# Performance work log

Hardware: AMD Instinct MI355X
Metric: run time of the kernel (lower is better)

Reference implementation:

```python
import jax, jax.numpy as jnp
import numpy as np

N_NODES = 100000
N_EDGES = 1600000
NUM_FEATURES = 32
EDGE_DIM = 8
GAT_DIM = 16
HEADS = 4
HID = GAT_DIM * HEADS  # 64
OUT_DIM = 2
NUM_GRAPHS = 64
NEG_SLOPE = 0.2


def setup_inputs() -> dict:
    key = jax.random.key(0)
    ks = jax.random.split(key, 24)
    g = lambda k, shp, fan: jax.random.normal(k, shp, jnp.float32) * (1.0 / np.sqrt(fan))
    inp = {
        'x': jax.random.normal(ks[0], (N_NODES, NUM_FEATURES), jnp.float32),
        'edge_index': jax.random.randint(ks[1], (2, N_EDGES), 0, N_NODES, jnp.int64),
        'edge_attr': jax.random.normal(ks[2], (N_EDGES, EDGE_DIM), jnp.float32),
        'batch': jnp.sort(jax.random.randint(ks[3], (N_NODES,), 0, NUM_GRAPHS, jnp.int64)),
        # input GATConv params (PyG: lin bias-free, att_* of shape [H,C], bias [H*C])
        'W0': g(ks[4], (NUM_FEATURES, HID), NUM_FEATURES),
        'att_src0': g(ks[5], (HEADS, GAT_DIM), GAT_DIM),
        'att_dst0': g(ks[6], (HEADS, GAT_DIM), GAT_DIM),
        'We0': g(ks[7], (EDGE_DIM, HID), EDGE_DIM),
        'att_e0': g(ks[8], (HEADS, GAT_DIM), GAT_DIM),
        'b0': jnp.zeros((HID,), jnp.float32),
        # 2 hidden GATConv layers, stacked on a leading layer axis
        'Wh': g(ks[9], (2, HID, HID), HID),
        'att_src_h': g(ks[10], (2, HEADS, GAT_DIM), GAT_DIM),
        'att_dst_h': g(ks[11], (2, HEADS, GAT_DIM), GAT_DIM),
        'We_h': g(ks[12], (2, EDGE_DIM, HID), EDGE_DIM),
        'att_e_h': g(ks[13], (2, HEADS, GAT_DIM), GAT_DIM),
        'bh': jnp.zeros((2, HID), jnp.float32),
        # MLP head
        'fc1_w': g(ks[14], (HID, 2 * GAT_DIM), HID),
        'fc1_b': jnp.zeros((2 * GAT_DIM,), jnp.float32),
        'fc2_w': g(ks[15], (2 * GAT_DIM, OUT_DIM), 2 * GAT_DIM),
        'fc2_b': jnp.zeros((OUT_DIM,), jnp.float32),
    }
    return inp


def _gat_conv(x, src, dst, ea, W, a_s, a_d, We, a_e, b, n_nodes):
    # x: [N, Fin] -> out: [N, H*C]
    xp = (x @ W).reshape(n_nodes, HEADS, GAT_DIM)
    al_s = jnp.einsum('nhc,hc->nh', xp, a_s)            # per-node src logits
    al_d = jnp.einsum('nhc,hc->nh', xp, a_d)
    ep = (ea @ We).reshape(-1, HEADS, GAT_DIM)
    al_e = jnp.einsum('ehc,hc->eh', ep, a_e)
    alpha = jax.nn.leaky_relu(al_s[src] + al_d[dst] + al_e, NEG_SLOPE)  # [E,H]
    m = jax.ops.segment_max(alpha, dst, num_segments=n_nodes)
    m = jnp.where(jnp.isfinite(m), m, 0.0)              # nodes with no in-edges
    ex = jnp.exp(alpha - m[dst])
    den = jax.ops.segment_sum(ex, dst, num_segments=n_nodes)
    coef = ex / (den[dst] + 1e-16)                      # segment softmax over dst
    out = jax.ops.segment_sum(xp[src] * coef[..., None], dst, num_segments=n_nodes)
    return out.reshape(n_nodes, HID) + b


def _forward(x, edge_index, edge_attr, batch, W0, att_src0, att_dst0, We0, att_e0,
             b0, Wh, att_src_h, att_dst_h, We_h, att_e_h, bh, fc1_w, fc1_b, fc2_w, fc2_b):
    n = x.shape[0]
    src, dst = edge_index[0], edge_index[1]
    # PyG add_self_loops(fill_value='mean'): self-loop attr = mean of incoming edge attrs
    cnt = jax.ops.segment_sum(jnp.ones((src.shape[0],), x.dtype), dst, num_segments=n)
    mean_attr = jax.ops.segment_sum(edge_attr, dst, num_segments=n) / jnp.clip(cnt, 1.0)[:, None]
    loop = jnp.arange(n, dtype=src.dtype)
    src_sl = jnp.concatenate([src, loop])
    dst_sl = jnp.concatenate([dst, loop])
    ea_sl = jnp.concatenate([edge_attr, mean_attr], axis=0)

    h = _gat_conv(x, src_sl, dst_sl, ea_sl, W0, att_src0, att_dst0, We0, att_e0, b0, n)
    h = jax.nn.relu(h)
    for i in range(2):  # source has `x - F.relu(x)` (no-op): no ReLU between hidden layers
        h = _gat_conv(h, src_sl, dst_sl, ea_sl, Wh[i], att_src_h[i], att_dst_h[i],
                      We_h[i], att_e_h[i], bh[i], n)
    # global_mean_pool over graphs
    ones = jnp.ones((n,), h.dtype)
    gcnt = jax.ops.segment_sum(ones, batch, num_segments=NUM_GRAPHS)
    pooled = jax.ops.segment_sum(h, batch, num_segments=NUM_GRAPHS) / jnp.clip(gcnt, 1.0)[:, None]
    y = jax.nn.relu(pooled @ fc1_w + fc1_b)
    return y @ fc2_w + fc2_b


def reference(x, edge_index, edge_attr, batch, W0, att_src0, att_dst0, We0, att_e0,
              b0, Wh, att_src_h, att_dst_h, We_h, att_e_h, bh, fc1_w, fc1_b, fc2_w, fc2_b):
    return _forward(x, edge_index, edge_attr, batch, W0, att_src0, att_dst0, We0, att_e0,
                    b0, Wh, att_src_h, att_dst_h, We_h, att_e_h, bh, fc1_w, fc1_b, fc2_w, fc2_b)
```

## Files before the change

kernel.cpp:

```cpp
#include <hip/hip_runtime.h>
#include <hip/hip_bf16.h>
#include <hip/hip_fp16.h>

#define N_NODES 100000
#define N_EDGES 1600000
#define E_SL (N_EDGES + N_NODES)
#define HID 64
#define NUM_GRAPHS 64
#define NEG_SLOPE 0.2f
#define SCAN_CHUNK 1024
#define SCAN_NB ((N_NODES + SCAN_CHUNK - 1) / SCAN_CHUNK)
#define ROW_W 8
#define XP_NODES_PER_BLK 16
#define POOL_NODES_PER_BLK 256
#define BUILD_NB (N_EDGES / 128)
#define XP0_NB ((N_NODES + 15) / 16)


__global__ void hist_kernel(const int* __restrict__ ei, int* __restrict__ cnt,
                            int* __restrict__ rank) {
    int e = blockIdx.x * blockDim.x + threadIdx.x;
    if (e >= N_EDGES) return;
    rank[e] = atomicAdd(&cnt[ei[N_EDGES + e]], 1);
}

__global__ void scan_local_kernel(const int* __restrict__ cnt, int* __restrict__ row_ptr,
                                  int* __restrict__ bsum) {
    __shared__ int s[256];
    int t = threadIdx.x;
    int base = blockIdx.x * SCAN_CHUNK + t * 4;
    int v[4]; int sum = 0;
    #pragma unroll
    for (int i = 0; i < 4; ++i) {
        int idx = base + i;
        v[i] = (idx < N_NODES) ? cnt[idx] + 1 : 0;
        sum += v[i];
    }
    s[t] = sum;
    __syncthreads();
    for (int off = 1; off < 256; off <<= 1) {
        int x = (t >= off) ? s[t - off] : 0;
        __syncthreads();
        s[t] += x;
        __syncthreads();
    }
    int run = s[t] - sum;
    #pragma unroll
    for (int i = 0; i < 4; ++i) {
        int idx = base + i;
        if (idx < N_NODES) row_ptr[idx] = run;
        run += v[i];
    }
    if (t == 255) bsum[blockIdx.x] = s[255];
}

__global__ void scan_bsum_kernel(int* __restrict__ bsum) {
    if (threadIdx.x != 0) return;
    int acc = 0;
    for (int i = 0; i < SCAN_NB; ++i) { int v = bsum[i]; bsum[i] = acc; acc += v; }
}

__global__ void scan_add_kernel(int* __restrict__ row_ptr, const int* __restrict__ bsum) {
    int i = blockIdx.x * blockDim.x + threadIdx.x;
    if (i > N_NODES) return;
    if (i == N_NODES) row_ptr[i] = E_SL;
    else row_ptr[i] += bsum[i >> 10];
}

__global__ void weff_all_kernel(const float* __restrict__ We0, const float* __restrict__ ae0,
                                const float* __restrict__ Weh, const float* __restrict__ aeh,
                                float* __restrict__ weff) {
    int t = threadIdx.x;
    if (t >= 96) return;
    int layer = t >> 5, r = t & 31;
    int dd = r >> 2, h = r & 3;
    const float* We = (layer == 0) ? We0 : Weh + (size_t)(layer - 1) * 8 * 64;
    const float* ae = (layer == 0) ? ae0 : aeh + (size_t)(layer - 1) * 64;
    float s = 0.f;
    #pragma unroll
    for (int c = 0; c < 16; ++c) s += We[dd * 64 + h * 16 + c] * ae[h * 16 + c];
    weff[layer * 32 + dd * 4 + h] = s;
}

__global__ __launch_bounds__(256) void build_xp0_kernel(
    const int* __restrict__ ei, const float* __restrict__ ea,
    const int* __restrict__ row_ptr, const int* __restrict__ rank,
    const float* __restrict__ weff, unsigned int* __restrict__ ale_csr,
    const float* __restrict__ x, const float* __restrict__ W0,
    const float* __restrict__ a_s, const float* __restrict__ a_d,
    __half* __restrict__ xp, float* __restrict__ als, float* __restrict__ ald) {
    int b = blockIdx.x;
    int g = b / 3, r3 = b - g * 3;
    if (r3 == 2) {
        int wave = threadIdx.x >> 6, lane = threadIdx.x & 63;
        float wcol[32];
        #pragma unroll
        for (int k = 0; k < 32; ++k) wcol[k] = W0[k * 64 + lane];
        float asl = a_s[lane], adl = a_d[lane];
        int n0 = g * XP_NODES_PER_BLK + wave * 4;
        #pragma unroll 1
        for (int ni = 0; ni < 4; ++ni) {
            int n = n0 + ni;
            if (n >= N_NODES) return;
            const float* xr = x + (size_t)n * 32;
            float a0 = 0.f, a1 = 0.f, a2 = 0.f, a3 = 0.f;
            #pragma unroll
            for (int k = 0; k < 32; k += 4) {
                float4 xv = *(const float4*)(xr + k);
                a0 += xv.x * wcol[k];     a1 += xv.y * wcol[k + 1];
                a2 += xv.z * wcol[k + 2]; a3 += xv.w * wcol[k + 3];
            }
            float acc = (a0 + a1) + (a2 + a3);
            xp[(size_t)n * 64 + lane] = __float2half(acc);
            float ps = acc * asl, pd = acc * adl;
            #pragma unroll
            for (int mk = 8; mk >= 1; mk >>= 1) {
                ps += __shfl_xor(ps, mk, 16);
                pd += __shfl_xor(pd, mk, 16);
            }
            if ((lane & 15) == 0) {
                als[(size_t)n * 4 + (lane >> 4)] = ps;
                ald[(size_t)n * 4 + (lane >> 4)] = pd;
            }
        }
        return;
    }
    int build_b = g * 2 + r3;
    int e = build_b * 128 + (threadIdx.x >> 1);
    int q = threadIdx.x & 1;
    int d = ei[N_EDGES + e];
    float4 a = *((const float4*)(ea + (size_t)e * 8) + q);
    float o0 = __shfl_xor(a.x, 1), o1 = __shfl_xor(a.y, 1);
    float o2 = __shfl_xor(a.z, 1), o3 = __shfl_xor(a.w, 1);
    float av[8];
    av[0] = q ? o0 : a.x;  av[1] = q ? o1 : a.y;
    av[2] = q ? o2 : a.z;  av[3] = q ? o3 : a.w;
    av[4] = q ? a.x : o0;  av[5] = q ? a.y : o1;
    av[6] = q ? a.z : o2;  av[7] = q ? a.w : o3;
    unsigned int w[4];
    if (q == 0) {
        float al[8];
        #pragma unroll
        for (int l = 0; l < 2; ++l) {
            #pragma unroll
            for (int h = 0; h < 4; ++h) {
                float s = 0.f;
                #pragma unroll
                for (int j = 0; j < 8; ++j) s += av[j] * weff[l * 32 + j * 4 + h];
                al[l * 4 + h] = s;
            }
        }
        __half2 p0 = __floats2half2_rn(al[0], al[1]);
        __half2 p1 = __floats2half2_rn(al[2], al[3]);
        __half2 p2 = __floats2half2_rn(al[4], al[5]);
        __half2 p3 = __floats2half2_rn(al[6], al[7]);
        w[0] = *(unsigned int*)&p0; w[1] = *(unsigned int*)&p1;
        w[2] = *(unsigned int*)&p2; w[3] = *(unsigned int*)&p3;
    } else {
        float al[4];
        #pragma unroll
        for (int h = 0; h < 4; ++h) {
            float s = 0.f;
            #pragma unroll
            for (int j = 0; j < 8; ++j) s += av[j] * weff[64 + j * 4 + h];
            al[h] = s;
        }
        __half2 p0 = __floats2half2_rn(al[0], al[1]);
        __half2 p1 = __floats2half2_rn(al[2], al[3]);
        w[0] = *(unsigned int*)&p0; w[1] = *(unsigned int*)&p1;
        w[2] = (unsigned int)ei[e];
        w[3] = 0u;
    }
    int pos = row_ptr[d] + rank[e];
    *(uint4*)(ale_csr + (size_t)pos * ROW_W + q * 4) =
        make_uint4(w[0], w[1], w[2], w[3]);
}

__global__ void mean_ea_kernel(const int* __restrict__ row_ptr,
                               unsigned int* __restrict__ ale_csr) {
    int idx = blockIdx.x * blockDim.x + threadIdx.x;
    if (idx >= N_NODES * 2) return;
    int n = idx >> 1, part = idx & 1;
    int start = row_ptr[n], last = row_ptr[n + 1] - 1;
    float inv = 1.f / fmaxf((float)(last - start), 1.f);
    if (part == 0) {
        float s[8] = {0.f, 0.f, 0.f, 0.f, 0.f, 0.f, 0.f, 0.f};
        for (int pos = start; pos < last; ++pos) {
            uint4 v = *(const uint4*)(ale_csr + (size_t)pos * ROW_W);
            float2 f0 = __half22float2(*(const __half2*)&v.x);
            float2 f1 = __half22float2(*(const __half2*)&v.y);
            float2 f2 = __half22float2(*(const __half2*)&v.z);
            float2 f3 = __half22float2(*(const __half2*)&v.w);
            s[0] += f0.x; s[1] += f0.y; s[2] += f1.x; s[3] += f1.y;
            s[4] += f2.x; s[5] += f2.y; s[6] += f3.x; s[7] += f3.y;
        }
        __half2 p0 = __floats2half2_rn(s[0] * inv, s[1] * inv);
        __half2 p1 = __floats2half2_rn(s[2] * inv, s[3] * inv);
        __half2 p2 = __floats2half2_rn(s[4] * inv, s[5] * inv);
        __half2 p3 = __floats2half2_rn(s[6] * inv, s[7] * inv);
        *(uint4*)(ale_csr + (size_t)last * ROW_W) =
            make_uint4(*(unsigned int*)&p0, *(unsigned int*)&p1,
                       *(unsigned int*)&p2, *(unsigned int*)&p3);
    } else {
        float s[4] = {0.f, 0.f, 0.f, 0.f};
        for (int pos = start; pos < last; ++pos) {
            uint2 v = *(const uint2*)(ale_csr + (size_t)pos * ROW_W + 4);
            float2 f0 = __half22float2(*(const __half2*)&v.x);
            float2 f1 = __half22float2(*(const __half2*)&v.y);
            s[0] += f0.x; s[1] += f0.y; s[2] += f1.x; s[3] += f1.y;
        }
        __half2 p0 = __floats2half2_rn(s[0] * inv, s[1] * inv);
        __half2 p1 = __floats2half2_rn(s[2] * inv, s[3] * inv);
        uint4 w = make_uint4(*(unsigned int*)&p0, *(unsigned int*)&p1,
                             (unsigned int)n, 0u);
        *(uint4*)(ale_csr + (size_t)last * ROW_W + 4) = w;
    }
}


template <int FIN>
__global__ __launch_bounds__(64) void xp_kernel(
    const float* __restrict__ xin, const float* __restrict__ W,
    const float* __restrict__ a_s, const float* __restrict__ a_d,
    __half* __restrict__ xp, float* __restrict__ als, float* __restrict__ ald) {
    int lane = threadIdx.x;
    float wcol[FIN];
    #pragma unroll
    for (int k = 0; k < FIN; ++k) wcol[k] = W[k * 64 + lane];
    float asl = a_s[lane], adl = a_d[lane];
    int n0 = blockIdx.x * XP_NODES_PER_BLK;
    #pragma unroll 1
    for (int ni = 0; ni < XP_NODES_PER_BLK; ++ni) {
        int n = n0 + ni;
        if (n >= N_NODES) return;
        const float* xr = xin + (size_t)n * FIN;
        float a0 = 0.f, a1 = 0.f, a2 = 0.f, a3 = 0.f;
        #pragma unroll
        for (int k = 0; k < FIN; k += 4) {
            float4 xv = *(const float4*)(xr + k);
            a0 += xv.x * wcol[k];     a1 += xv.y * wcol[k + 1];
            a2 += xv.z * wcol[k + 2]; a3 += xv.w * wcol[k + 3];
        }
        float acc = (a0 + a1) + (a2 + a3);
        xp[(size_t)n * 64 + lane] = __float2half(acc);
        float ps = acc * asl, pd = acc * adl;
        #pragma unroll
        for (int mk = 8; mk >= 1; mk >>= 1) {
            ps += __shfl_xor(ps, mk, 16);
            pd += __shfl_xor(pd, mk, 16);
        }
        if ((lane & 15) == 0) {
            als[(size_t)n * 4 + (lane >> 4)] = ps;
            ald[(size_t)n * 4 + (lane >> 4)] = pd;
        }
    }
}

__global__ __launch_bounds__(256) void gat_node_kernel(
    const int* __restrict__ row_ptr, const unsigned int* __restrict__ ale_csr,
    const float* __restrict__ als, const float* __restrict__ ald,
    const __half* __restrict__ xp, int layer,
    float* __restrict__ out, const float* __restrict__ bias, int relu_flag) {
    __shared__ float exl[4 * 256];
    __shared__ int   coll[4 * 64];
    int wave = threadIdx.x >> 6, lane = threadIdx.x & 63;
    int node = blockIdx.x * 4 + wave;
    if (node >= N_NODES) return;
    int start = row_ptr[node], end = row_ptr[node + 1];
    int deg = end - start;
    int wb = wave * 64, wb4 = wave * 256;
    int cq = lane & 15;
    int eg = lane >> 4;
    int hv = cq >> 2;

    float4 ad4 = *(const float4*)(ald + (size_t)node * 4);

    float4 acc4 = make_float4(0.f, 0.f, 0.f, 0.f);
    float csum = 0.f;

    for (int base = 0; base < deg; base += 64) {
        int cnt = min(64, deg - base);
        float ex0 = 0.f, ex1 = 0.f, ex2 = 0.f, ex3 = 0.f;
        int s = 0;
        if (lane < cnt) {
            const unsigned int* row = ale_csr + (size_t)(start + base + lane) * ROW_W;
            uint2 alew = *(const uint2*)(row + 2 * layer);
            s = (int)row[6];
            float2 e01 = __half22float2(*(const __half2*)&alew.x);
            float2 e23 = __half22float2(*(const __half2*)&alew.y);
            float4 as4 = *(const float4*)(als + (size_t)s * 4);
            float v0 = as4.x + ad4.x + e01.x;
            float v1 = as4.y + ad4.y + e01.y;
            float v2 = as4.z + ad4.z + e23.x;
            float v3 = as4.w + ad4.w + e23.y;
            ex0 = expf((v0 >= 0.f) ? v0 : NEG_SLOPE * v0);
            ex1 = expf((v1 >= 0.f) ? v1 : NEG_SLOPE * v1);
            ex2 = expf((v2 >= 0.f) ? v2 : NEG_SLOPE * v2);
            ex3 = expf((v3 >= 0.f) ? v3 : NEG_SLOPE * v3);
        }
        *(float4*)(exl + wb4 + lane * 4) = make_float4(ex0, ex1, ex2, ex3);
        coll[wb + lane] = s;
        const float* exw = exl + wb4 + hv;
        int cntUp = (cnt + 15) & ~15;
        for (int j = eg; j < cntUp; j += 16) {
            int s0 = coll[wb + j],     s1 = coll[wb + j + 4];
            int s2 = coll[wb + j + 8], s3 = coll[wb + j + 12];
            float c0 = exw[(j) * 4],      c1 = exw[(j + 4) * 4];
            float c2 = exw[(j + 8) * 4],  c3 = exw[(j + 12) * 4];
            uint2 x0 = *(const uint2*)(xp + (size_t)s0 * 64 + cq * 4);
            uint2 x1 = *(const uint2*)(xp + (size_t)s1 * 64 + cq * 4);
            uint2 x2 = *(const uint2*)(xp + (size_t)s2 * 64 + cq * 4);
            uint2 x3 = *(const uint2*)(xp + (size_t)s3 * 64 + cq * 4);
            float2 f00 = __half22float2(*(const __half2*)&x0.x);
            float2 f01 = __half22float2(*(const __half2*)&x0.y);
            float2 f10 = __half22float2(*(const __half2*)&x1.x);
            float2 f11 = __half22float2(*(const __half2*)&x1.y);
            float2 f20 = __half22float2(*(const __half2*)&x2.x);
            float2 f21 = __half22float2(*(const __half2*)&x2.y);
            float2 f30 = __half22float2(*(const __half2*)&x3.x);
            float2 f31 = __half22float2(*(const __half2*)&x3.y);
            acc4.x += c0 * f00.x + c1 * f10.x + c2 * f20.x + c3 * f30.x;
            acc4.y += c0 * f00.y + c1 * f10.y + c2 * f20.y + c3 * f30.y;
            acc4.z += c0 * f01.x + c1 * f11.x + c2 * f21.x + c3 * f31.x;
            acc4.w += c0 * f01.y + c1 * f11.y + c2 * f21.y + c3 * f31.y;
            csum   += c0 + c1 + c2 + c3;
        }
    }
    #pragma unroll
    for (int mk = 16; mk < 64; mk <<= 1) {
        acc4.x += __shfl_xor(acc4.x, mk);
        acc4.y += __shfl_xor(acc4.y, mk);
        acc4.z += __shfl_xor(acc4.z, mk);
        acc4.w += __shfl_xor(acc4.w, mk);
        csum   += __shfl_xor(csum, mk);
    }
    if (eg == 0) {
        float inv = 1.f / (csum + 1e-16f);
        float4 b4 = *(const float4*)(bias + cq * 4);
        float4 v;
        v.x = acc4.x * inv + b4.x;
        v.y = acc4.y * inv + b4.y;
        v.z = acc4.z * inv + b4.z;
        v.w = acc4.w * inv + b4.w;
        if (relu_flag) {
            v.x = fmaxf(v.x, 0.f); v.y = fmaxf(v.y, 0.f);
            v.z = fmaxf(v.z, 0.f); v.w = fmaxf(v.w, 0.f);
        }
        *(float4*)(out + (size_t)node * 64 + cq * 4) = v;
    }
}

__global__ void pool_kernel(const float* __restrict__ h, const int* __restrict__ batch,
                            float* __restrict__ pooled) {
    int base = blockIdx.x * POOL_NODES_PER_BLK;
    int tid = threadIdx.x;
    int c = tid & 63, r = tid >> 6;
    float acc = 0.f;
    int curg = -1;
    for (int i = r; i < POOL_NODES_PER_BLK; i += 4) {
        int n = base + i;
        if (n >= N_NODES) break;
        int g = batch[n];
        if (g != curg) {
            if (curg >= 0) atomicAdd(&pooled[curg * 64 + c], acc);
            curg = g; acc = 0.f;
        }
        acc += h[(size_t)n * 64 + c];
    }
    if (curg >= 0) atomicAdd(&pooled[curg * 64 + c], acc);
}

__global__ void mlp_kernel(const float* __restrict__ pooled, const int* __restrict__ batch,
                           const float* __restrict__ w1, const float* __restrict__ b1,
                           const float* __restrict__ w2, const float* __restrict__ b2,
                           float* __restrict__ y) {
    int g = blockIdx.x, t = threadIdx.x;
    __shared__ float p[64], f1[32];
    __shared__ float invc_s;
    if (t == 0) {
        int lo = 0, hi = N_NODES;
        while (lo < hi) { int mid = (lo + hi) >> 1; if (batch[mid] < g) lo = mid + 1; else hi = mid; }
        int start = lo;
        hi = N_NODES;
        while (lo < hi) { int mid = (lo + hi) >> 1; if (batch[mid] < g + 1) lo = mid + 1; else hi = mid; }
        invc_s = 1.f / fmaxf((float)(lo - start), 1.f);
    }
    __syncthreads();
    p[t] = pooled[g * 64 + t] * invc_s;
    __syncthreads();
    if (t < 32) {
        float a = b1[t];
        #pragma unroll
        for (int k = 0; k < 64; ++k) a += p[k] * w1[k * 32 + t];
        f1[t] = fmaxf(a, 0.f);
    }
    __syncthreads();
    if (t < 2) {
        float a = b2[t];
        #pragma unroll
        for (int k = 0; k < 32; ++k) a += f1[k] * w2[k * 2 + t];
        y[g * 2 + t] = a;
    }
}

extern "C" void kernel_launch(void* const* d_in, const int* in_sizes, int n_in,
                              void* d_out, int out_size, void* d_ws, size_t ws_size,
                              hipStream_t stream) {
    const float* x    = (const float*)d_in[0];
    const int*   ei   = (const int*)d_in[1];
    const float* ea   = (const float*)d_in[2];
    const int*   batch= (const int*)d_in[3];
    const float* W0   = (const float*)d_in[4];
    const float* as0  = (const float*)d_in[5];
    const float* ad0  = (const float*)d_in[6];
    const float* We0  = (const float*)d_in[7];
    const float* ae0  = (const float*)d_in[8];
    const float* b0   = (const float*)d_in[9];
    const float* Wh   = (const float*)d_in[10];
    const float* ash  = (const float*)d_in[11];
    const float* adh  = (const float*)d_in[12];
    const float* Weh  = (const float*)d_in[13];
    const float* aeh  = (const float*)d_in[14];
    const float* bh   = (const float*)d_in[15];
    const float* w1   = (const float*)d_in[16];
    const float* b1   = (const float*)d_in[17];
    const float* w2   = (const float*)d_in[18];
    const float* b2   = (const float*)d_in[19];
    float* out = (float*)d_out;

    char* wsb = (char*)d_ws;
    size_t off = 0;
    auto alloc = [&](size_t bytes) { char* p = wsb + off; off += (bytes + 255) & ~(size_t)255; return p; };
    int*          row_ptr = (int*)alloc((size_t)(N_NODES + 1) * 4);
    unsigned int* ale_csr = (unsigned int*)alloc((size_t)E_SL * ROW_W * 4);
    float*        als     = (float*)alloc((size_t)N_NODES * 4 * 4);
    float*        ald     = (float*)alloc((size_t)N_NODES * 4 * 4);
    float*        weff    = (float*)alloc(3 * 32 * 4);
    float*        pooled  = (float*)alloc((size_t)NUM_GRAPHS * 64 * 4);
    __half*       bufA    = (__half*)alloc((size_t)N_NODES * 64 * 2);
    float*        bufB    = (float*)alloc((size_t)N_NODES * 64 * 4);
    int* cnt  = (int*)bufB;
    int* bsum = cnt + N_NODES;
    int* rank = bsum + ((SCAN_NB + 63) & ~63);

    weff_all_kernel<<<1, 128, 0, stream>>>(We0, ae0, Weh, aeh, weff);
    hipMemsetAsync(cnt, 0, (size_t)N_NODES * 4, stream);
    hist_kernel<<<(N_EDGES + 255) / 256, 256, 0, stream>>>(ei, cnt, rank);
    scan_local_kernel<<<SCAN_NB, 256, 0, stream>>>(cnt, row_ptr, bsum);
    scan_bsum_kernel<<<1, 64, 0, stream>>>(bsum);
    scan_add_kernel<<<(N_NODES + 256) / 256, 256, 0, stream>>>(row_ptr, bsum);
    build_xp0_kernel<<<BUILD_NB + XP0_NB, 256, 0, stream>>>(
        ei, ea, row_ptr, rank, weff, ale_csr,
        x, W0, as0, ad0, bufA, als, ald);
    mean_ea_kernel<<<(N_NODES * 2 + 255) / 256, 256, 0, stream>>>(row_ptr, ale_csr);

    for (int layer = 0; layer < 3; ++layer) {
        const float *bb;
        int relu_flag = (layer == 0);
        if (layer == 0) {
            bb = b0;
        } else {
            int i = layer - 1;
            const float* W   = Wh  + (size_t)i * 64 * 64;
            const float* as_ = ash + (size_t)i * 64;
            const float* ad_ = adh + (size_t)i * 64;
            bb  = bh  + (size_t)i * 64;
            int xpgrid = (N_NODES + XP_NODES_PER_BLK - 1) / XP_NODES_PER_BLK;
            xp_kernel<64><<<xpgrid, 64, 0, stream>>>(bufB, W, as_, ad_, bufA, als, ald);
        }
        gat_node_kernel<<<(N_NODES + 3) / 4, 256, 0, stream>>>(
            row_ptr, ale_csr, als, ald, bufA, layer, bufB, bb, relu_flag);
    }
    hipMemsetAsync(pooled, 0, (size_t)NUM_GRAPHS * 64 * 4, stream);
    pool_kernel<<<(N_NODES + POOL_NODES_PER_BLK - 1) / POOL_NODES_PER_BLK, 256, 0, stream>>>(
        bufB, batch, pooled);
    mlp_kernel<<<NUM_GRAPHS, 64, 0, stream>>>(pooled, batch, w1, b1, w2, b2, out);
}
```

Measured before the change: 616.0 us.

## Fuse next-layer node projection into GAT aggregation epilogue with ping-pong buffers

Removes the separate xp_kernel launches for the two hidden layers. Each GAT aggregation kernel now computes the next layer's projection, fp16 xp and attention logits in its epilogue, staging the aggregated row in shared memory. Ping-pong buffers for xp/als/ald keep the fused writes from racing with reads of the current layer. This avoids writing and re-reading the fp32 hidden activations and cuts two launches, at the cost of extra per-wave matvec work and register pressure in the gather kernel. The bounds check in build_xp0 is also dropped and its inner loop unrolled by two, relying on N_NODES being divisible by 16.

```diff
diff --git a/kernel.cpp b/kernel.cpp
--- a/kernel.cpp
+++ b/kernel.cpp
@@ -14,7 +14,7 @@
 #define XP_NODES_PER_BLK 16
 #define POOL_NODES_PER_BLK 256
 #define BUILD_NB (N_EDGES / 128)
-#define XP0_NB ((N_NODES + 15) / 16)
+#define XP0_NB (N_NODES / 16)
 
 
 __global__ void hist_kernel(const int* __restrict__ ei, int* __restrict__ cnt,
@@ -98,10 +98,9 @@
         for (int k = 0; k < 32; ++k) wcol[k] = W0[k * 64 + lane];
         float asl = a_s[lane], adl = a_d[lane];
         int n0 = g * XP_NODES_PER_BLK + wave * 4;
-        #pragma unroll 1
+        #pragma unroll 2
         for (int ni = 0; ni < 4; ++ni) {
             int n = n0 + ni;
-            if (n >= N_NODES) return;
             const float* xr = x + (size_t)n * 32;
             float a0 = 0.f, a1 = 0.f, a2 = 0.f, a3 = 0.f;
             #pragma unroll
@@ -217,52 +216,18 @@
     }
 }
 
-
-template <int FIN>
-__global__ __launch_bounds__(64) void xp_kernel(
-    const float* __restrict__ xin, const float* __restrict__ W,
-    const float* __restrict__ a_s, const float* __restrict__ a_d,
-    __half* __restrict__ xp, float* __restrict__ als, float* __restrict__ ald) {
-    int lane = threadIdx.x;
-    float wcol[FIN];
-    #pragma unroll
-    for (int k = 0; k < FIN; ++k) wcol[k] = W[k * 64 + lane];
-    float asl = a_s[lane], adl = a_d[lane];
-    int n0 = blockIdx.x * XP_NODES_PER_BLK;
-    #pragma unroll 1
-    for (int ni = 0; ni < XP_NODES_PER_BLK; ++ni) {
-        int n = n0 + ni;
-        if (n >= N_NODES) return;
-        const float* xr = xin + (size_t)n * FIN;
-        float a0 = 0.f, a1 = 0.f, a2 = 0.f, a3 = 0.f;
-        #pragma unroll
-        for (int k = 0; k < FIN; k += 4) {
-            float4 xv = *(const float4*)(xr + k);
-            a0 += xv.x * wcol[k];     a1 += xv.y * wcol[k + 1];
-            a2 += xv.z * wcol[k + 2]; a3 += xv.w * wcol[k + 3];
-        }
-        float acc = (a0 + a1) + (a2 + a3);
-        xp[(size_t)n * 64 + lane] = __float2half(acc);
-        float ps = acc * asl, pd = acc * adl;
-        #pragma unroll
-        for (int mk = 8; mk >= 1; mk >>= 1) {
-            ps += __shfl_xor(ps, mk, 16);
-            pd += __shfl_xor(pd, mk, 16);
-        }
-        if ((lane & 15) == 0) {
-            als[(size_t)n * 4 + (lane >> 4)] = ps;
-            ald[(size_t)n * 4 + (lane >> 4)] = pd;
-        }
-    }
-}
-
+template <bool FUSE_XP>
 __global__ __launch_bounds__(256) void gat_node_kernel(
     const int* __restrict__ row_ptr, const unsigned int* __restrict__ ale_csr,
     const float* __restrict__ als, const float* __restrict__ ald,
     const __half* __restrict__ xp, int layer,
-    float* __restrict__ out, const float* __restrict__ bias, int relu_flag) {
+    float* __restrict__ out, const float* __restrict__ bias, int relu_flag,
+    const float* __restrict__ Wn, const float* __restrict__ asn,
+    const float* __restrict__ adn, __half* __restrict__ xpn,
+    float* __restrict__ alsn, float* __restrict__ aldn) {
     __shared__ float exl[4 * 256];
     __shared__ int   coll[4 * 64];
+    __shared__ float hrow[4 * 64];
     int wave = threadIdx.x >> 6, lane = threadIdx.x & 63;
     int node = blockIdx.x * 4 + wave;
     if (node >= N_NODES) return;
@@ -334,19 +299,42 @@
         acc4.w += __shfl_xor(acc4.w, mk);
         csum   += __shfl_xor(csum, mk);
     }
-    if (eg == 0) {
-        float inv = 1.f / (csum + 1e-16f);
-        float4 b4 = *(const float4*)(bias + cq * 4);
-        float4 v;
-        v.x = acc4.x * inv + b4.x;
-        v.y = acc4.y * inv + b4.y;
-        v.z = acc4.z * inv + b4.z;
-        v.w = acc4.w * inv + b4.w;
-        if (relu_flag) {
-            v.x = fmaxf(v.x, 0.f); v.y = fmaxf(v.y, 0.f);
-            v.z = fmaxf(v.z, 0.f); v.w = fmaxf(v.w, 0.f);
-        }
-        *(float4*)(out + (size_t)node * 64 + cq * 4) = v;
+    float inv = 1.f / (csum + 1e-16f);
+    float4 b4 = *(const float4*)(bias + cq * 4);
+    float4 v;
+    v.x = acc4.x * inv + b4.x;
+    v.y = acc4.y * inv + b4.y;
+    v.z = acc4.z * inv + b4.z;
+    v.w = acc4.w * inv + b4.w;
+    if (relu_flag) {
+        v.x = fmaxf(v.x, 0.f); v.y = fmaxf(v.y, 0.f);
+        v.z = fmaxf(v.z, 0.f); v.w = fmaxf(v.w, 0.f);
+    }
+    if (!FUSE_XP) {
+        if (eg == 0)
+            *(float4*)(out + (size_t)node * 64 + cq * 4) = v;
+    } else {
+        if (eg == 0) *(float4*)(hrow + wb + cq * 4) = v;
+        float acc = 0.f;
+        #pragma unroll
+        for (int k0 = 0; k0 < 64; k0 += 8) {
+            float wv[8];
+            #pragma unroll
+            for (int j = 0; j < 8; ++j) wv[j] = Wn[(k0 + j) * 64 + lane];
+            #pragma unroll
+            for (int j = 0; j < 8; ++j) acc += hrow[wb + k0 + j] * wv[j];
+        }
+        xpn[(size_t)node * 64 + lane] = __float2half(acc);
+        float ps = acc * asn[lane], pd = acc * adn[lane];
+        #pragma unroll
+        for (int mk = 8; mk >= 1; mk >>= 1) {
+            ps += __shfl_xor(ps, mk, 16);
+            pd += __shfl_xor(pd, mk, 16);
+        }
+        if ((lane & 15) == 0) {
+            alsn[(size_t)node * 4 + (lane >> 4)] = ps;
+            aldn[(size_t)node * 4 + (lane >> 4)] = pd;
+        }
     }
 }
 
@@ -433,15 +421,22 @@
     auto alloc = [&](size_t bytes) { char* p = wsb + off; off += (bytes + 255) & ~(size_t)255; return p; };
     int*          row_ptr = (int*)alloc((size_t)(N_NODES + 1) * 4);
     unsigned int* ale_csr = (unsigned int*)alloc((size_t)E_SL * ROW_W * 4);
-    float*        als     = (float*)alloc((size_t)N_NODES * 4 * 4);
-    float*        ald     = (float*)alloc((size_t)N_NODES * 4 * 4);
+    float*        als0_b  = (float*)alloc((size_t)N_NODES * 4 * 4);
+    float*        ald0_b  = (float*)alloc((size_t)N_NODES * 4 * 4);
+    float*        als1_b  = (float*)alloc((size_t)N_NODES * 4 * 4);
+    float*        ald1_b  = (float*)alloc((size_t)N_NODES * 4 * 4);
     float*        weff    = (float*)alloc(3 * 32 * 4);
     float*        pooled  = (float*)alloc((size_t)NUM_GRAPHS * 64 * 4);
-    __half*       bufA    = (__half*)alloc((size_t)N_NODES * 64 * 2);
+    __half*       xpb0    = (__half*)alloc((size_t)N_NODES * 64 * 2);
+    __half*       xpb1    = (__half*)alloc((size_t)N_NODES * 64 * 2);
     float*        bufB    = (float*)alloc((size_t)N_NODES * 64 * 4);
     int* cnt  = (int*)bufB;
     int* bsum = cnt + N_NODES;
     int* rank = bsum + ((SCAN_NB + 63) & ~63);
+
+    float* alsb[2] = {als0_b, als1_b};
+    float* aldb[2] = {ald0_b, ald1_b};
+    __half* xpb[2] = {xpb0, xpb1};
 
     weff_all_kernel<<<1, 128, 0, stream>>>(We0, ae0, Weh, aeh, weff);
     hipMemsetAsync(cnt, 0, (size_t)N_NODES * 4, stream);
@@ -451,26 +446,23 @@
     scan_add_kernel<<<(N_NODES + 256) / 256, 256, 0, stream>>>(row_ptr, bsum);
     build_xp0_kernel<<<BUILD_NB + XP0_NB, 256, 0, stream>>>(
         ei, ea, row_ptr, rank, weff, ale_csr,
-        x, W0, as0, ad0, bufA, als, ald);
+        x, W0, as0, ad0, xpb[0], alsb[0], aldb[0]);
     mean_ea_kernel<<<(N_NODES * 2 + 255) / 256, 256, 0, stream>>>(row_ptr, ale_csr);
 
-    for (int layer = 0; layer < 3; ++layer) {
-        const float *bb;
-        int relu_flag = (layer == 0);
-        if (layer == 0) {
-            bb = b0;
-        } else {
-            int i = layer - 1;
-            const float* W   = Wh  + (size_t)i * 64 * 64;
-            const float* as_ = ash + (size_t)i * 64;
-            const float* ad_ = adh + (size_t)i * 64;
-            bb  = bh  + (size_t)i * 64;
-            int xpgrid = (N_NODES + XP_NODES_PER_BLK - 1) / XP_NODES_PER_BLK;
-            xp_kernel<64><<<xpgrid, 64, 0, stream>>>(bufB, W, as_, ad_, bufA, als, ald);
-        }
-        gat_node_kernel<<<(N_NODES + 3) / 4, 256, 0, stream>>>(
-            row_ptr, ale_csr, als, ald, bufA, layer, bufB, bb, relu_flag);
-    }
+    int gat_grid = (N_NODES + 3) / 4;
+    gat_node_kernel<true><<<gat_grid, 256, 0, stream>>>(
+        row_ptr, ale_csr, alsb[0], aldb[0], xpb[0], 0,
+        nullptr, b0, 1,
+        Wh, ash, adh, xpb[1], alsb[1], aldb[1]);
+    gat_node_kernel<true><<<gat_grid, 256, 0, stream>>>(
+        row_ptr, ale_csr, alsb[1], aldb[1], xpb[1], 1,
+        nullptr, bh, 0,
+        Wh + (size_t)64 * 64, ash + 64, adh + 64, xpb[0], alsb[0], aldb[0]);
+    gat_node_kernel<false><<<gat_grid, 256, 0, stream>>>(
+        row_ptr, ale_csr, alsb[0], aldb[0], xpb[0], 2,
+        bufB, bh + 64, 0,
+        nullptr, nullptr, nullptr, nullptr, nullptr, nullptr);
+
     hipMemsetAsync(pooled, 0, (size_t)NUM_GRAPHS * 64 * 4, stream);
     pool_kernel<<<(N_NODES + POOL_NODES_PER_BLK - 1) / POOL_NODES_PER_BLK, 256, 0, stream>>>(
         bufB, batch, pooled);
```

Result: no change. 615.0 us (-0.2%).
